# Kernel optimization log

Hardware: AMD Instinct MI355X
Metric: run time of the kernel (lower is better)

The kernel has to match this reference:

```python
import jax, jax.numpy as jnp
import numpy as np
from jax.scipy.special import logsumexp

SCALE = 10.0
EPS = 1e-05
MARGIN_INTRA = 40.0
MARGIN_INTER = 6.0
K_INTRA = 4   # sorted1[4:]
K_INTER = 6   # sorted2[6:]


def setup_inputs() -> dict:
    key = jax.random.key(0)
    k1, k2 = jax.random.split(key)
    n, d, n_cams = 4096, 256, 8
    feature = jax.random.normal(k1, (n, d), dtype=jnp.float32)
    camid = jax.random.randint(k2, (n,), 0, n_cams, dtype=jnp.int64)
    return {"feature": feature, "camid": camid}


def reference(feature, camid):
    n = feature.shape[0]
    # pairwise Euclidean distances: ||fi||^2 + ||fj||^2 - 2 fi.fj + eps, clamped, sqrt
    sq = jnp.sum(feature * feature, axis=1)                      # [n]
    dist = sq[:, None] + sq[None, :] + EPS - 2.0 * (feature @ feature.T)
    dist = jnp.sqrt(jnp.clip(dist, 1e-12))                       # [n, n]

    same_cam = camid[:, None] == camid[None, :]                  # [n, n] bool
    inf = jnp.array(jnp.inf, dtype=dist.dtype)

    # masked sorts: +inf padding sorts to the end and contributes exp(-inf)=0
    sorted_intra = jnp.sort(jnp.where(same_cam, dist, inf), axis=1)   # [n, n]
    sorted_inter = jnp.sort(jnp.where(same_cam, inf, dist), axis=1)   # [n, n]

    # x = log(sum(exp(-scale * sorted[:1]))) == -scale * sorted[0]
    x_intra = -SCALE * sorted_intra[:, 0]
    y_intra = logsumexp(-SCALE * sorted_intra[:, K_INTRA:], axis=1)
    x_inter = -SCALE * sorted_inter[:, 0]
    y_inter = logsumexp(-SCALE * sorted_inter[:, K_INTER:], axis=1)

    loss_intra = jnp.sum(jnp.maximum(-x_intra + y_intra + MARGIN_INTRA, 0.0))
    loss_inter = jnp.sum(jnp.maximum(-x_inter + y_inter + MARGIN_INTER, 0.0))
    return (loss_intra + 0.5 * loss_inter) / n
```

## Files before the change

### kernel.cpp

```cpp
#include <hip/hip_runtime.h>
#include <hip/hip_bf16.h>
#include <math.h>

#define N 4096
#define D 256
#define SCALEF 10.0f
#define EPSF 1e-5f
#define MARGIN_INTRA 40.0f
#define MARGIN_INTER 6.0f
#define LI 3
#define LX 6
#define NCHUNK 16
#define NSTRIP 32
#define PPARTS (NCHUNK * 2)

typedef unsigned short ushort_t;
typedef __attribute__((ext_vector_type(8))) short short8;
typedef __attribute__((ext_vector_type(4))) float floatx4;

__device__ __forceinline__ ushort_t f2bf(float x) {
    __hip_bfloat16 h = __float2bfloat16(x);
    return *reinterpret_cast<ushort_t*>(&h);
}
__device__ __forceinline__ float bf2f(ushort_t u) {
    __hip_bfloat16 h = *reinterpret_cast<__hip_bfloat16*>(&u);
    return __bfloat162float(h);
}

template <int L>
__device__ __forceinline__ void bubble_insert(float (&t)[L], float v) {
#pragma unroll
    for (int q = 0; q < L; ++q) {
        float hi = fmaxf(t[q], v);
        v = fminf(t[q], v);
        t[q] = hi;
    }
}

__global__ __launch_bounds__(64) void prep_kernel(const float* __restrict__ F,
                                                  ushort_t* __restrict__ Fhi,
                                                  ushort_t* __restrict__ Flo,
                                                  float* __restrict__ sq,
                                                  float* __restrict__ Rrow) {
    int row = blockIdx.x;
    int lane = threadIdx.x;
    float4 v = ((const float4*)(F + (size_t)row * D))[lane];
    ushort4 h, l;
    h.x = f2bf(v.x); l.x = f2bf(v.x - bf2f(h.x));
    h.y = f2bf(v.y); l.y = f2bf(v.y - bf2f(h.y));
    h.z = f2bf(v.z); l.z = f2bf(v.z - bf2f(h.z));
    h.w = f2bf(v.w); l.w = f2bf(v.w - bf2f(h.w));
    ((ushort4*)(Fhi + (size_t)row * D))[lane] = h;
    ((ushort4*)(Flo + (size_t)row * D))[lane] = l;
    float s = v.x * v.x + v.y * v.y + v.z * v.z + v.w * v.w;
#pragma unroll
    for (int off = 32; off > 0; off >>= 1) s += __shfl_down(s, off, 64);
    if (lane == 0) {
        sq[row] = s;
        Rrow[row] = -SCALEF * sqrtf(2.0f * s);
    }
}

#define LDST 40

__global__ __launch_bounds__(256, 2) void fused_kernel(
    const ushort_t* __restrict__ Fhi, const ushort_t* __restrict__ Flo,
    const float* __restrict__ sq, const float* __restrict__ Rrow,
    const int* __restrict__ camid,
    float4* __restrict__ partA, float4* __restrict__ partB, float4* __restrict__ partC) {
    __shared__ ushort_t lds[4][128 * LDST];
    int tid = threadIdx.x;
    int wave = tid >> 6, lane = tid & 63;
    int wr = wave >> 1, wc = wave & 1;
    int lane15 = lane & 15, quad = lane >> 4;
    int cid = blockIdx.x, sid = blockIdx.y;
    int i0 = sid * 128, j00 = cid * 256;

    float si[4], Ri4[4];
    int ci4[4], ig[4];
#pragma unroll
    for (int ni = 0; ni < 4; ++ni) {
        int i = i0 + wc * 64 + ni * 16 + lane15;
        ig[ni] = i;
        si[ni] = sq[i];
        Ri4[ni] = Rrow[i];
        ci4[ni] = camid[i];
    }

    float tI[4][LI], tX[4][LX], sIa[4], sXa[4];
#pragma unroll
    for (int ni = 0; ni < 4; ++ni) {
#pragma unroll
        for (int q = 0; q < LI; ++q) tI[ni][q] = -INFINITY;
#pragma unroll
        for (int q = 0; q < LX; ++q) tX[ni][q] = -INFINITY;
        sIa[ni] = 0.0f; sXa[ni] = 0.0f;
    }

    int srow = tid >> 1, shalf = tid & 1;
    const ushort_t* gBh = Fhi + (size_t)(i0 + srow) * D + shalf * 16;
    const ushort_t* gBl = Flo + (size_t)(i0 + srow) * D + shalf * 16;
    ushort_t* sdst = &lds[0][0] + srow * LDST + shalf * 16;

#pragma unroll 1
    for (int jt = 0; jt < 2; ++jt) {
        int j0 = j00 + jt * 128;
        const ushort_t* gAh = Fhi + (size_t)(j0 + srow) * D + shalf * 16;
        const ushort_t* gAl = Flo + (size_t)(j0 + srow) * D + shalf * 16;
        floatx4 acc[4][4] = {};

#pragma unroll 1
        for (int kt = 0; kt < 8; ++kt) {
            int koff = kt * 32;
            short8 ra[2], rb[2], rc[2], rd[2];
#pragma unroll
            for (int q = 0; q < 2; ++q) {
                ra[q] = *(const short8*)(gAh + koff + q * 8);
                rb[q] = *(const short8*)(gAl + koff + q * 8);
                rc[q] = *(const short8*)(gBh + koff + q * 8);
                rd[q] = *(const short8*)(gBl + koff + q * 8);
            }
            __syncthreads();
#pragma unroll
            for (int q = 0; q < 2; ++q) {
                *(short8*)(sdst + 0 * 128 * LDST + q * 8) = ra[q];
                *(short8*)(sdst + 1 * 128 * LDST + q * 8) = rb[q];
                *(short8*)(sdst + 2 * 128 * LDST + q * 8) = rc[q];
                *(short8*)(sdst + 3 * 128 * LDST + q * 8) = rd[q];
            }
            __syncthreads();

            short8 ahi[4], alo[4], bhi[4], blo[4];
            int eoff = quad * 8;
#pragma unroll
            for (int mi = 0; mi < 4; ++mi) {
                int r = wr * 64 + mi * 16 + lane15;
                ahi[mi] = *(const short8*)(&lds[0][0] + r * LDST + eoff);
                alo[mi] = *(const short8*)(&lds[1][0] + r * LDST + eoff);
            }
#pragma unroll
            for (int ni = 0; ni < 4; ++ni) {
                int r = wc * 64 + ni * 16 + lane15;
                bhi[ni] = *(const short8*)(&lds[2][0] + r * LDST + eoff);
                blo[ni] = *(const short8*)(&lds[3][0] + r * LDST + eoff);
            }
#pragma unroll
            for (int mi = 0; mi < 4; ++mi)
#pragma unroll
                for (int ni = 0; ni < 4; ++ni) {
                    acc[mi][ni] = __builtin_amdgcn_mfma_f32_16x16x32_bf16(ahi[mi], bhi[ni], acc[mi][ni], 0, 0, 0);
                    acc[mi][ni] = __builtin_amdgcn_mfma_f32_16x16x32_bf16(ahi[mi], blo[ni], acc[mi][ni], 0, 0, 0);
                    acc[mi][ni] = __builtin_amdgcn_mfma_f32_16x16x32_bf16(alo[mi], bhi[ni], acc[mi][ni], 0, 0, 0);
                }
        }

#pragma unroll
        for (int mi = 0; mi < 4; ++mi) {
            int jg0 = j0 + wr * 64 + mi * 16 + quad * 4;
            float4 sj4 = *(const float4*)(sq + jg0);
            int4 cj4 = *(const int4*)(camid + jg0);
            const float* sjp = (const float*)&sj4;
            const int* cjp = (const int*)&cj4;
#pragma unroll
            for (int ni = 0; ni < 4; ++ni) {
                int dd = jg0 - ig[ni];
#pragma unroll
                for (int r = 0; r < 4; ++r) {
                    float d2 = si[ni] + sjp[r] + EPSF - 2.0f * acc[mi][ni][r];
                    float d = sqrtf(fmaxf(d2, 1e-12f));
                    float x = -SCALEF * d;
                    float e = __expf(x - Ri4[ni]);
                    bool ii = (cjp[r] == ci4[ni]);
                    bool dg = ((dd + r) == 0);
                    bool okI = ii && !dg;
                    sIa[ni] += okI ? e : 0.0f;
                    sXa[ni] += ii ? 0.0f : e;
                    bubble_insert<LI>(tI[ni], okI ? x : -INFINITY);
                    bubble_insert<LX>(tX[ni], ii ? -INFINITY : x);
                }
            }
        }
    }

#pragma unroll
    for (int off = 16; off <= 32; off <<= 1) {
#pragma unroll
        for (int ni = 0; ni < 4; ++ni) {
            sIa[ni] += __shfl_xor(sIa[ni], off, 64);
            sXa[ni] += __shfl_xor(sXa[ni], off, 64);
            float oI[LI], oX[LX];
#pragma unroll
            for (int q = 0; q < LI; ++q) oI[q] = __shfl_xor(tI[ni][q], off, 64);
#pragma unroll
            for (int q = 0; q < LX; ++q) oX[q] = __shfl_xor(tX[ni][q], off, 64);
#pragma unroll
            for (int q = 0; q < LI; ++q) bubble_insert<LI>(tI[ni], oI[q]);
#pragma unroll
            for (int q = 0; q < LX; ++q) bubble_insert<LX>(tX[ni], oX[q]);
        }
    }

    if (quad == 0) {
        int p = cid * 2 + wr;
#pragma unroll
        for (int ni = 0; ni < 4; ++ni) {
            size_t idx = (size_t)p * N + ig[ni];
            partA[idx] = make_float4(tI[ni][0], tI[ni][1], tI[ni][2], sIa[ni]);
            partB[idx] = make_float4(tX[ni][0], tX[ni][1], tX[ni][2], tX[ni][3]);
            partC[idx] = make_float4(tX[ni][4], tX[ni][5], sXa[ni], 0.0f);
        }
    }
}

__global__ __launch_bounds__(256) void merge_kernel(const float4* __restrict__ partA,
                                                    const float4* __restrict__ partB,
                                                    const float4* __restrict__ partC,
                                                    const float* __restrict__ Rrow,
                                                    float* __restrict__ rowloss) {
    int row = blockIdx.x * 256 + threadIdx.x;
    float mI[LI] = {-INFINITY, -INFINITY, -INFINITY};
    float mX[LX] = {-INFINITY, -INFINITY, -INFINITY, -INFINITY, -INFINITY, -INFINITY};
    float SI = 0.0f, SX = 0.0f;
#pragma unroll 1
    for (int p = 0; p < PPARTS; ++p) {
        size_t idx = (size_t)p * N + row;
        float4 a = partA[idx];
        float4 b = partB[idx];
        float4 c = partC[idx];
        bubble_insert<LI>(mI, a.x); bubble_insert<LI>(mI, a.y); bubble_insert<LI>(mI, a.z);
        SI += a.w;
        bubble_insert<LX>(mX, b.x); bubble_insert<LX>(mX, b.y);
        bubble_insert<LX>(mX, b.z); bubble_insert<LX>(mX, b.w);
        bubble_insert<LX>(mX, c.x); bubble_insert<LX>(mX, c.y);
        SX += c.z;
    }
    float R = Rrow[row];
    float subI = __expf(mI[0] - R) + __expf(mI[1] - R) + __expf(mI[2] - R);
    float restI = fmaxf(SI - subI, 1e-37f);
    float yI = R + logf(restI);
    float hI = fmaxf(yI + SCALEF * sqrtf(EPSF) + MARGIN_INTRA, 0.0f);
    float subX = __expf(mX[0] - R) + __expf(mX[1] - R) + __expf(mX[2] - R) +
                 __expf(mX[3] - R) + __expf(mX[4] - R) + __expf(mX[5] - R);
    float restX = fmaxf(SX - subX, 1e-37f);
    float yX = R + logf(restX);
    float hX = fmaxf(-mX[0] + yX + MARGIN_INTER, 0.0f);
    rowloss[row] = hI + 0.5f * hX;
}

__global__ __launch_bounds__(256) void final_reduce(const float* __restrict__ rowloss,
                                                    float* __restrict__ out) {
    __shared__ float sbuf[256];
    int tid = threadIdx.x;
    float acc = 0.0f;
#pragma unroll
    for (int s = 0; s < 16; ++s) acc += rowloss[tid + s * 256];
    sbuf[tid] = acc;
    __syncthreads();
    for (int stride = 128; stride > 0; stride >>= 1) {
        if (tid < stride) sbuf[tid] += sbuf[tid + stride];
        __syncthreads();
    }
    if (tid == 0) out[0] = sbuf[0] * (1.0f / (float)N);
}

extern "C" void kernel_launch(void* const* d_in, const int* in_sizes, int n_in,
                              void* d_out, int out_size, void* d_ws, size_t ws_size,
                              hipStream_t stream) {
    const float* F = (const float*)d_in[0];
    const int* camid = (const int*)d_in[1];
    float* out = (float*)d_out;
    char* ws = (char*)d_ws;

    ushort_t* Fhi = (ushort_t*)ws;
    ushort_t* Flo = Fhi + (size_t)N * D;
    float* sq = (float*)(ws + 2 * (size_t)N * D * 2);
    float* Rrow = sq + N;
    float* rowloss = Rrow + N;
    float4* partA = (float4*)(ws + 2 * (size_t)N * D * 2 + 3 * N * 4);
    float4* partB = partA + (size_t)PPARTS * N;
    float4* partC = partB + (size_t)PPARTS * N;

    prep_kernel<<<N, 64, 0, stream>>>(F, Fhi, Flo, sq, Rrow);
    fused_kernel<<<dim3(NCHUNK, NSTRIP), 256, 0, stream>>>(Fhi, Flo, sq, Rrow, camid,
                                                           partA, partB, partC);
    merge_kernel<<<N / 256, 256, 0, stream>>>(partA, partB, partC, Rrow, rowloss);
    final_reduce<<<1, 256, 0, stream>>>(rowloss, out);
}
```

Before: 130.3 us.

## Sort rows by camera and specialize cross-camera tiles, fuse final reduction

A new kernel permutes rows so they are grouped by camera id. Tiles whose row and column camera ranges do not overlap then take a simplified epilogue that skips the camid compares and the intra-camera top-k. The grid is reshaped to 128x128 tiles with higher occupancy, sqrt uses the hardware intrinsic, and the final reduce is folded into the merge kernel via atomicAdd. This adds a single-block permutation kernel and doubles the partial buffers the merge must read.

Measured after the change: 164.0 us. +25.9%, slower.

```diff
diff --git a/kernel.cpp b/kernel.cpp
--- a/kernel.cpp
+++ b/kernel.cpp
@@ -10,13 +10,17 @@
 #define MARGIN_INTER 6.0f
 #define LI 3
 #define LX 6
-#define NCHUNK 16
-#define NSTRIP 32
-#define PPARTS (NCHUNK * 2)
+#define NJB 32
+#define NIB 32
+#define PPARTS (NJB * 2)
 
 typedef unsigned short ushort_t;
 typedef __attribute__((ext_vector_type(8))) short short8;
 typedef __attribute__((ext_vector_type(4))) float floatx4;
+
+__device__ __forceinline__ float fast_sqrtf(float x) {
+    return __builtin_amdgcn_sqrtf(x);
+}
 
 __device__ __forceinline__ ushort_t f2bf(float x) {
     __hip_bfloat16 h = __float2bfloat16(x);
@@ -37,14 +41,48 @@
     }
 }
 
+__global__ __launch_bounds__(512) void perm_kernel(const int* __restrict__ camid,
+                                                   int* __restrict__ perm,
+                                                   int* __restrict__ camid_s,
+                                                   float* __restrict__ out) {
+    __shared__ int counts[8];
+    int wave = threadIdx.x >> 6, lane = threadIdx.x & 63;
+    if (threadIdx.x == 0) out[0] = 0.0f;
+    int cnt = 0;
+#pragma unroll 1
+    for (int c = 0; c < N / 64; ++c) {
+        int v = camid[c * 64 + lane];
+        unsigned long long m = __ballot(v == wave);
+        cnt += __popcll(m);
+    }
+    if (lane == 0) counts[wave] = cnt;
+    __syncthreads();
+    int base = 0;
+    for (int c = 0; c < wave; ++c) base += counts[c];
+#pragma unroll 1
+    for (int c = 0; c < N / 64; ++c) {
+        int idx = c * 64 + lane;
+        int v = camid[idx];
+        unsigned long long m = __ballot(v == wave);
+        if (v == wave) {
+            int pre = __popcll(m & ((1ull << lane) - 1ull));
+            perm[base + pre] = idx;
+            camid_s[base + pre] = wave;
+        }
+        base += __popcll(m);
+    }
+}
+
 __global__ __launch_bounds__(64) void prep_kernel(const float* __restrict__ F,
+                                                  const int* __restrict__ perm,
                                                   ushort_t* __restrict__ Fhi,
                                                   ushort_t* __restrict__ Flo,
                                                   float* __restrict__ sq,
                                                   float* __restrict__ Rrow) {
     int row = blockIdx.x;
+    int orig = perm[row];
     int lane = threadIdx.x;
-    float4 v = ((const float4*)(F + (size_t)row * D))[lane];
+    float4 v = ((const float4*)(F + (size_t)orig * D))[lane];
     ushort4 h, l;
     h.x = f2bf(v.x); l.x = f2bf(v.x - bf2f(h.x));
     h.y = f2bf(v.y); l.y = f2bf(v.y - bf2f(h.y));
@@ -63,10 +101,10 @@
 
 #define LDST 40
 
-__global__ __launch_bounds__(256, 2) void fused_kernel(
+__global__ __launch_bounds__(256, 3) void fused_kernel(
     const ushort_t* __restrict__ Fhi, const ushort_t* __restrict__ Flo,
     const float* __restrict__ sq, const float* __restrict__ Rrow,
-    const int* __restrict__ camid,
+    const int* __restrict__ camid_s,
     float4* __restrict__ partA, float4* __restrict__ partB, float4* __restrict__ partC) {
     __shared__ ushort_t lds[4][128 * LDST];
     int tid = threadIdx.x;
@@ -74,7 +112,11 @@
     int wr = wave >> 1, wc = wave & 1;
     int lane15 = lane & 15, quad = lane >> 4;
     int cid = blockIdx.x, sid = blockIdx.y;
-    int i0 = sid * 128, j00 = cid * 256;
+    int i0 = sid * 128, j0 = cid * 128;
+
+    int ci_lo = camid_s[i0], ci_hi = camid_s[i0 + 127];
+    int cj_lo = camid_s[j0], cj_hi = camid_s[j0 + 127];
+    bool disjoint = (ci_hi < cj_lo) || (cj_hi < ci_lo);
 
     float si[4], Ri4[4];
     int ci4[4], ig[4];
@@ -84,7 +126,7 @@
         ig[ni] = i;
         si[ni] = sq[i];
         Ri4[ni] = Rrow[i];
-        ci4[ni] = camid[i];
+        ci4[ni] = camid_s[i];
     }
 
     float tI[4][LI], tX[4][LX], sIa[4], sXa[4];
@@ -98,77 +140,93 @@
     }
 
     int srow = tid >> 1, shalf = tid & 1;
+    const ushort_t* gAh = Fhi + (size_t)(j0 + srow) * D + shalf * 16;
+    const ushort_t* gAl = Flo + (size_t)(j0 + srow) * D + shalf * 16;
     const ushort_t* gBh = Fhi + (size_t)(i0 + srow) * D + shalf * 16;
     const ushort_t* gBl = Flo + (size_t)(i0 + srow) * D + shalf * 16;
     ushort_t* sdst = &lds[0][0] + srow * LDST + shalf * 16;
 
+    floatx4 acc[4][4] = {};
+
 #pragma unroll 1
-    for (int jt = 0; jt < 2; ++jt) {
-        int j0 = j00 + jt * 128;
-        const ushort_t* gAh = Fhi + (size_t)(j0 + srow) * D + shalf * 16;
-        const ushort_t* gAl = Flo + (size_t)(j0 + srow) * D + shalf * 16;
-        floatx4 acc[4][4] = {};
-
-#pragma unroll 1
-        for (int kt = 0; kt < 8; ++kt) {
-            int koff = kt * 32;
-            short8 ra[2], rb[2], rc[2], rd[2];
-#pragma unroll
-            for (int q = 0; q < 2; ++q) {
-                ra[q] = *(const short8*)(gAh + koff + q * 8);
-                rb[q] = *(const short8*)(gAl + koff + q * 8);
-                rc[q] = *(const short8*)(gBh + koff + q * 8);
-                rd[q] = *(const short8*)(gBl + koff + q * 8);
+    for (int kt = 0; kt < 8; ++kt) {
+        int koff = kt * 32;
+        short8 ra[2], rb[2], rc[2], rd[2];
+#pragma unroll
+        for (int q = 0; q < 2; ++q) {
+            ra[q] = *(const short8*)(gAh + koff + q * 8);
+            rb[q] = *(const short8*)(gAl + koff + q * 8);
+            rc[q] = *(const short8*)(gBh + koff + q * 8);
+            rd[q] = *(const short8*)(gBl + koff + q * 8);
+        }
+        __syncthreads();
+#pragma unroll
+        for (int q = 0; q < 2; ++q) {
+            *(short8*)(sdst + 0 * 128 * LDST + q * 8) = ra[q];
+            *(short8*)(sdst + 1 * 128 * LDST + q * 8) = rb[q];
+            *(short8*)(sdst + 2 * 128 * LDST + q * 8) = rc[q];
+            *(short8*)(sdst + 3 * 128 * LDST + q * 8) = rd[q];
+        }
+        __syncthreads();
+
+        short8 ahi[4], alo[4], bhi[4], blo[4];
+        int eoff = quad * 8;
+#pragma unroll
+        for (int mi = 0; mi < 4; ++mi) {
+            int r = wr * 64 + mi * 16 + lane15;
+            ahi[mi] = *(const short8*)(&lds[0][0] + r * LDST + eoff);
+            alo[mi] = *(const short8*)(&lds[1][0] + r * LDST + eoff);
+        }
+#pragma unroll
+        for (int ni = 0; ni < 4; ++ni) {
+            int r = wc * 64 + ni * 16 + lane15;
+            bhi[ni] = *(const short8*)(&lds[2][0] + r * LDST + eoff);
+            blo[ni] = *(const short8*)(&lds[3][0] + r * LDST + eoff);
+        }
+#pragma unroll
+        for (int mi = 0; mi < 4; ++mi)
+#pragma unroll
+            for (int ni = 0; ni < 4; ++ni) {
+                acc[mi][ni] = __builtin_amdgcn_mfma_f32_16x16x32_bf16(ahi[mi], bhi[ni], acc[mi][ni], 0, 0, 0);
+                acc[mi][ni] = __builtin_amdgcn_mfma_f32_16x16x32_bf16(ahi[mi], blo[ni], acc[mi][ni], 0, 0, 0);
+                acc[mi][ni] = __builtin_amdgcn_mfma_f32_16x16x32_bf16(alo[mi], bhi[ni], acc[mi][ni], 0, 0, 0);
             }
-            __syncthreads();
-#pragma unroll
-            for (int q = 0; q < 2; ++q) {
-                *(short8*)(sdst + 0 * 128 * LDST + q * 8) = ra[q];
-                *(short8*)(sdst + 1 * 128 * LDST + q * 8) = rb[q];
-                *(short8*)(sdst + 2 * 128 * LDST + q * 8) = rc[q];
-                *(short8*)(sdst + 3 * 128 * LDST + q * 8) = rd[q];
-            }
-            __syncthreads();
-
-            short8 ahi[4], alo[4], bhi[4], blo[4];
-            int eoff = quad * 8;
-#pragma unroll
-            for (int mi = 0; mi < 4; ++mi) {
-                int r = wr * 64 + mi * 16 + lane15;
-                ahi[mi] = *(const short8*)(&lds[0][0] + r * LDST + eoff);
-                alo[mi] = *(const short8*)(&lds[1][0] + r * LDST + eoff);
-            }
-#pragma unroll
-            for (int ni = 0; ni < 4; ++ni) {
-                int r = wc * 64 + ni * 16 + lane15;
-                bhi[ni] = *(const short8*)(&lds[2][0] + r * LDST + eoff);
-                blo[ni] = *(const short8*)(&lds[3][0] + r * LDST + eoff);
-            }
-#pragma unroll
-            for (int mi = 0; mi < 4; ++mi)
-#pragma unroll
-                for (int ni = 0; ni < 4; ++ni) {
-                    acc[mi][ni] = __builtin_amdgcn_mfma_f32_16x16x32_bf16(ahi[mi], bhi[ni], acc[mi][ni], 0, 0, 0);
-                    acc[mi][ni] = __builtin_amdgcn_mfma_f32_16x16x32_bf16(ahi[mi], blo[ni], acc[mi][ni], 0, 0, 0);
-                    acc[mi][ni] = __builtin_amdgcn_mfma_f32_16x16x32_bf16(alo[mi], bhi[ni], acc[mi][ni], 0, 0, 0);
-                }
-        }
-
+    }
+
+    if (disjoint) {
 #pragma unroll
         for (int mi = 0; mi < 4; ++mi) {
             int jg0 = j0 + wr * 64 + mi * 16 + quad * 4;
             float4 sj4 = *(const float4*)(sq + jg0);
-            int4 cj4 = *(const int4*)(camid + jg0);
+            const float* sjp = (const float*)&sj4;
+#pragma unroll
+            for (int ni = 0; ni < 4; ++ni) {
+                float sb = si[ni] + EPSF;
+#pragma unroll
+                for (int r = 0; r < 4; ++r) {
+                    float d2 = fmaxf(fmaf(-2.0f, acc[mi][ni][r], sb + sjp[r]), 1e-12f);
+                    float x = -SCALEF * fast_sqrtf(d2);
+                    sXa[ni] += __expf(x - Ri4[ni]);
+                    bubble_insert<LX>(tX[ni], x);
+                }
+            }
+        }
+    } else {
+#pragma unroll
+        for (int mi = 0; mi < 4; ++mi) {
+            int jg0 = j0 + wr * 64 + mi * 16 + quad * 4;
+            float4 sj4 = *(const float4*)(sq + jg0);
+            int4 cj4 = *(const int4*)(camid_s + jg0);
             const float* sjp = (const float*)&sj4;
             const int* cjp = (const int*)&cj4;
 #pragma unroll
             for (int ni = 0; ni < 4; ++ni) {
                 int dd = jg0 - ig[ni];
+                float sb = si[ni] + EPSF;
 #pragma unroll
                 for (int r = 0; r < 4; ++r) {
-                    float d2 = si[ni] + sjp[r] + EPSF - 2.0f * acc[mi][ni][r];
-                    float d = sqrtf(fmaxf(d2, 1e-12f));
-                    float x = -SCALEF * d;
+                    float d2 = fmaxf(fmaf(-2.0f, acc[mi][ni][r], sb + sjp[r]), 1e-12f);
+                    float x = -SCALEF * fast_sqrtf(d2);
                     float e = __expf(x - Ri4[ni]);
                     bool ii = (cjp[r] == ci4[ni]);
                     bool dg = ((dd + r) == 0);
@@ -216,8 +274,10 @@
                                                     const float4* __restrict__ partB,
                                                     const float4* __restrict__ partC,
                                                     const float* __restrict__ Rrow,
-                                                    float* __restrict__ rowloss) {
-    int row = blockIdx.x * 256 + threadIdx.x;
+                                                    float* __restrict__ out) {
+    __shared__ float sbuf[256];
+    int tid = threadIdx.x;
+    int row = blockIdx.x * 256 + tid;
     float mI[LI] = {-INFINITY, -INFINITY, -INFINITY};
     float mX[LX] = {-INFINITY, -INFINITY, -INFINITY, -INFINITY, -INFINITY, -INFINITY};
     float SI = 0.0f, SX = 0.0f;
@@ -244,23 +304,13 @@
     float restX = fmaxf(SX - subX, 1e-37f);
     float yX = R + logf(restX);
     float hX = fmaxf(-mX[0] + yX + MARGIN_INTER, 0.0f);
-    rowloss[row] = hI + 0.5f * hX;
-}
-
-__global__ __launch_bounds__(256) void final_reduce(const float* __restrict__ rowloss,
-                                                    float* __restrict__ out) {
-    __shared__ float sbuf[256];
-    int tid = threadIdx.x;
-    float acc = 0.0f;
-#pragma unroll
-    for (int s = 0; s < 16; ++s) acc += rowloss[tid + s * 256];
-    sbuf[tid] = acc;
+    sbuf[tid] = hI + 0.5f * hX;
     __syncthreads();
     for (int stride = 128; stride > 0; stride >>= 1) {
         if (tid < stride) sbuf[tid] += sbuf[tid + stride];
         __syncthreads();
     }
-    if (tid == 0) out[0] = sbuf[0] * (1.0f / (float)N);
+    if (tid == 0) atomicAdd(out, sbuf[0] * (1.0f / (float)N));
 }
 
 extern "C" void kernel_launch(void* const* d_in, const int* in_sizes, int n_in,
@@ -275,14 +325,15 @@
     ushort_t* Flo = Fhi + (size_t)N * D;
     float* sq = (float*)(ws + 2 * (size_t)N * D * 2);
     float* Rrow = sq + N;
-    float* rowloss = Rrow + N;
-    float4* partA = (float4*)(ws + 2 * (size_t)N * D * 2 + 3 * N * 4);
+    int* perm = (int*)(Rrow + N);
+    int* camid_s = perm + N;
+    float4* partA = (float4*)(ws + 2 * (size_t)N * D * 2 + 4 * N * 4);
     float4* partB = partA + (size_t)PPARTS * N;
     float4* partC = partB + (size_t)PPARTS * N;
 
-    prep_kernel<<<N, 64, 0, stream>>>(F, Fhi, Flo, sq, Rrow);
-    fused_kernel<<<dim3(NCHUNK, NSTRIP), 256, 0, stream>>>(Fhi, Flo, sq, Rrow, camid,
-                                                           partA, partB, partC);
-    merge_kernel<<<N / 256, 256, 0, stream>>>(partA, partB, partC, Rrow, rowloss);
-    final_reduce<<<1, 256, 0, stream>>>(rowloss, out);
-}
+    perm_kernel<<<1, 512, 0, stream>>>(camid, perm, camid_s, out);
+    prep_kernel<<<N, 64, 0, stream>>>(F, perm, Fhi, Flo, sq, Rrow);
+    fused_kernel<<<dim3(NJB, NIB), 256, 0, stream>>>(Fhi, Flo, sq, Rrow, camid_s,
+                                                     partA, partB, partC);
+    merge_kernel<<<N / 256, 256, 0, stream>>>(partA, partB, partC, Rrow, out);
+}
```
